# Optimization experiments

Measured on AMD Instinct MI355X. Metric: run time of the kernel, lower is better.

Reference implementation:

```python
import jax, jax.numpy as jnp
import numpy as np


def quantize_ternary(w):
    # BitNet b1.58: scale by mean |w|, round, clamp to {-1,0,1}
    gamma = jnp.maximum(jnp.mean(jnp.abs(w)), 1e-8)
    return jnp.clip(jnp.round(w / gamma), -1.0, 1.0)


def setup_inputs() -> dict:
    key = jax.random.key(0)
    k1, k2, k3 = jax.random.split(key, 3)
    in_features, out_features = 4096, 4096
    x = jax.random.normal(k1, (4, 2048, in_features), dtype=jnp.float32)
    # kaiming_uniform-like init
    bound_w = 1.0 / np.sqrt(in_features)
    weight = jax.random.uniform(k2, (out_features, in_features), dtype=jnp.float32,
                                minval=-bound_w * np.sqrt(3.0), maxval=bound_w * np.sqrt(3.0))
    bias = jax.random.uniform(k3, (out_features,), dtype=jnp.float32,
                              minval=-bound_w, maxval=bound_w)
    return {"x": x, "weight": weight, "bias": bias}


def reference(x, weight, bias):
    qw = quantize_ternary(weight)  # [out, in], values in {-1,0,1}
    # F.linear: x @ qw.T + bias
    return jnp.einsum('bsi,oi->bso', x, qw) + bias
```

## Files before the change

### kernel.cpp

```cpp
#include <hip/hip_runtime.h>
#include <stdint.h>

#define M_DIM 8192
#define N_DIM 4096
#define K_DIM 4096
#define BM 256
#define BN 256
#define BKS 64
#define NSLAB (K_DIM / BKS)
#define SLOT_BYTES (256 * BKS)

typedef int i32x4 __attribute__((ext_vector_type(4)));

__device__ __forceinline__ void async_copy16(const void* g, void* l) {
    __builtin_amdgcn_global_load_lds(
        (const __attribute__((address_space(1))) void*)g,
        (__attribute__((address_space(3))) void*)l, 16, 0, 0);
}

__global__ __launch_bounds__(256) void abssum_partial(const float4* __restrict__ w,
                                                      double* __restrict__ partials) {
    const int lane = threadIdx.x & 63;
    const int wave = threadIdx.x >> 6;
    int base = blockIdx.x * 4096 + threadIdx.x;
    float s = 0.f;
    #pragma unroll
    for (int i = 0; i < 16; i++) {
        float4 v = w[base + i * 256];
        s += fabsf(v.x) + fabsf(v.y) + fabsf(v.z) + fabsf(v.w);
    }
    double d = (double)s;
    #pragma unroll
    for (int off = 32; off > 0; off >>= 1) d += __shfl_down(d, off, 64);
    __shared__ double wsum[4];
    if (lane == 0) wsum[wave] = d;
    __syncthreads();
    if (threadIdx.x == 0)
        partials[blockIdx.x] = (wsum[0] + wsum[1]) + (wsum[2] + wsum[3]);
}

__global__ __launch_bounds__(256) void gamma_reduce(const double* __restrict__ partials,
                                                    float* __restrict__ gamma_out) {
    const int lane = threadIdx.x & 63;
    const int wave = threadIdx.x >> 6;
    double d = partials[threadIdx.x] + partials[threadIdx.x + 256] +
               partials[threadIdx.x + 512] + partials[threadIdx.x + 768];
    #pragma unroll
    for (int off = 32; off > 0; off >>= 1) d += __shfl_down(d, off, 64);
    __shared__ double wsum[4];
    if (lane == 0) wsum[wave] = d;
    __syncthreads();
    if (threadIdx.x == 0) {
        double total = (wsum[0] + wsum[1]) + (wsum[2] + wsum[3]);
        float g = (float)(total * (1.0 / 16777216.0));
        gamma_out[0] = fmaxf(g, 1e-8f);
    }
}

__global__ __launch_bounds__(256) void wquant(const float4* __restrict__ w,
                                              char4* __restrict__ qw,
                                              const float* __restrict__ gamma_p, int n4) {
    float gamma = gamma_p[0];
    int i = blockIdx.x * blockDim.x + threadIdx.x;
    if (i >= n4) return;
    float4 v = w[i];
    char4 o;
    o.x = (signed char)fminf(fmaxf(rintf(v.x / gamma), -1.f), 1.f);
    o.y = (signed char)fminf(fmaxf(rintf(v.y / gamma), -1.f), 1.f);
    o.z = (signed char)fminf(fmaxf(rintf(v.z / gamma), -1.f), 1.f);
    o.w = (signed char)fminf(fmaxf(rintf(v.w / gamma), -1.f), 1.f);
    qw[i] = o;
}

__global__ __launch_bounds__(256) void xquant(const float4* __restrict__ x,
                                              char4* __restrict__ xq,
                                              float* __restrict__ xscale) {
    const int row = blockIdx.x;
    const int lane = threadIdx.x & 63;
    const int wave = threadIdx.x >> 6;
    const float4* xr = x + (size_t)row * (K_DIM / 4);
    float4 v[4];
    float m = 0.f;
    #pragma unroll
    for (int i = 0; i < 4; i++) {
        v[i] = xr[threadIdx.x + i * 256];
        m = fmaxf(m, fmaxf(fmaxf(fabsf(v[i].x), fabsf(v[i].y)),
                           fmaxf(fabsf(v[i].z), fabsf(v[i].w))));
    }
    #pragma unroll
    for (int off = 32; off > 0; off >>= 1) m = fmaxf(m, __shfl_down(m, off, 64));
    __shared__ float wmax[4];
    if (lane == 0) wmax[wave] = m;
    __syncthreads();
    const float mx = fmaxf(fmaxf(wmax[0], wmax[1]), fmaxf(wmax[2], wmax[3]));
    const float scale = fmaxf(mx * (1.f / 127.f), 1e-30f);
    const float inv = 1.f / scale;
    if (threadIdx.x == 0) xscale[row] = scale;
    char4* oq = xq + (size_t)row * (K_DIM / 4);
    #pragma unroll
    for (int i = 0; i < 4; i++) {
        char4 o;
        o.x = (signed char)fminf(fmaxf(rintf(v[i].x * inv), -127.f), 127.f);
        o.y = (signed char)fminf(fmaxf(rintf(v[i].y * inv), -127.f), 127.f);
        o.z = (signed char)fminf(fmaxf(rintf(v[i].z * inv), -127.f), 127.f);
        o.w = (signed char)fminf(fmaxf(rintf(v[i].w * inv), -127.f), 127.f);
        oq[threadIdx.x + i * 256] = o;
    }
}

__global__ __launch_bounds__(512, 2) void gemm_kernel(
    const char* __restrict__ xq,
    const char* __restrict__ qw,
    const float* __restrict__ xscale,
    const float* __restrict__ bias,
    float* __restrict__ out)
{
    __shared__ __align__(16) char As[4][SLOT_BYTES];
    __shared__ __align__(16) char Bs[4][SLOT_BYTES];

    const int tid  = threadIdx.x;
    const int wave = tid >> 6;
    const int lane = tid & 63;
    const int wm   = (wave >> 2) * 128;
    const int wn   = (wave & 3) * 64;
    const int lm   = lane & 15;
    const int q4   = lane >> 4;

    const int bm = blockIdx.y * BM;
    const int bn = blockIdx.x * BN;

    const int rsub = lane >> 2;
    const int csw  = (lane & 3) ^ ((lane >> 3) & 3);
    const char* gA[2];
    const char* gB[2];
    int ldsOff[2];
    #pragma unroll
    for (int j = 0; j < 2; j++) {
        const int r = wave * 32 + j * 16 + rsub;
        gA[j] = xq + (size_t)(bm + r) * K_DIM + csw * 16;
        gB[j] = qw + (size_t)(bn + r) * K_DIM + csw * 16;
        ldsOff[j] = (wave * 32 + j * 16) * BKS;
    }

    i32x4 acc[8][4];
    #pragma unroll
    for (int i = 0; i < 8; i++)
        #pragma unroll
        for (int j = 0; j < 4; j++) acc[i][j] = (i32x4){0, 0, 0, 0};

    const int pc = (q4 ^ ((lm >> 1) & 3)) * 16;

    auto stage_slab = [&](int ts, int slot) {
        async_copy16(gA[0] + (size_t)ts * BKS, &As[slot][ldsOff[0]]);
        async_copy16(gB[0] + (size_t)ts * BKS, &Bs[slot][ldsOff[0]]);
        async_copy16(gA[1] + (size_t)ts * BKS, &As[slot][ldsOff[1]]);
        async_copy16(gB[1] + (size_t)ts * BKS, &Bs[slot][ldsOff[1]]);
    };

    auto compute_slab = [&](const char* Ab, const char* Bb) {
        i32x4 b[4], a[8];
        #pragma unroll
        for (int ni = 0; ni < 4; ni++)
            b[ni] = *(const i32x4*)(Bb + (wn + ni * 16 + lm) * BKS + pc);
        #pragma unroll
        for (int mi = 0; mi < 8; mi++)
            a[mi] = *(const i32x4*)(Ab + (wm + mi * 16 + lm) * BKS + pc);
        __builtin_amdgcn_s_setprio(1);
        #pragma unroll
        for (int mi = 0; mi < 8; mi++)
            #pragma unroll
            for (int ni = 0; ni < 4; ni++)
                acc[mi][ni] = __builtin_amdgcn_mfma_i32_16x16x64_i8(
                    a[mi], b[ni], acc[mi][ni], 0, 0, 0);
        __builtin_amdgcn_s_setprio(0);
    };

    #pragma unroll
    for (int s = 0; s < 3; s++) stage_slab(s, s);
    asm volatile("s_waitcnt vmcnt(8)" ::: "memory");
    __builtin_amdgcn_s_barrier();

    for (int tb = 0; tb < NSLAB - 4; tb += 4) {
        #pragma unroll
        for (int u = 0; u < 4; u++) {
            stage_slab(tb + u + 3, (u + 3) & 3);
            compute_slab(As[u], Bs[u]);
            asm volatile("s_waitcnt vmcnt(8)" ::: "memory");
            __builtin_amdgcn_s_barrier();
        }
    }

    stage_slab(63, 3);
    compute_slab(As[0], Bs[0]);
    asm volatile("s_waitcnt vmcnt(8)" ::: "memory");
    __builtin_amdgcn_s_barrier();

    compute_slab(As[1], Bs[1]);
    asm volatile("s_waitcnt vmcnt(4)" ::: "memory");
    __builtin_amdgcn_s_barrier();

    compute_slab(As[2], Bs[2]);
    asm volatile("s_waitcnt vmcnt(0)" ::: "memory");
    __builtin_amdgcn_s_barrier();

    compute_slab(As[3], Bs[3]);

    float bl[4];
    #pragma unroll
    for (int ni = 0; ni < 4; ni++) bl[ni] = bias[bn + wn + ni * 16 + lm];

    #pragma unroll
    for (int mi = 0; mi < 8; mi++) {
        #pragma unroll
        for (int r = 0; r < 4; r++) {
            const int grow = bm + wm + mi * 16 + q4 * 4 + r;
            const float sc = xscale[grow];
            float* orow = out + (size_t)grow * N_DIM + bn + wn;
            #pragma unroll
            for (int ni = 0; ni < 4; ni++)
                orow[ni * 16 + lm] = sc * (float)acc[mi][ni][r] + bl[ni];
        }
    }
}

extern "C" void kernel_launch(void* const* d_in, const int* in_sizes, int n_in,
                              void* d_out, int out_size, void* d_ws, size_t ws_size,
                              hipStream_t stream) {
    const float* x    = (const float*)d_in[0];
    const float* w    = (const float*)d_in[1];
    const float* bias = (const float*)d_in[2];
    float* out = (float*)d_out;

    char* ws = (char*)d_ws;
    char*   xq       = ws;
    char*   qw       = ws + (size_t)M_DIM * K_DIM;
    float*  xscale   = (float*)(qw + (size_t)N_DIM * K_DIM);
    double* partials = (double*)(xscale + M_DIM);
    float*  gamma_p  = (float*)(partials + 1024);

    const int wn4 = (N_DIM * K_DIM) / 4;

    abssum_partial<<<1024, 256, 0, stream>>>((const float4*)w, partials);
    gamma_reduce<<<1, 256, 0, stream>>>(partials, gamma_p);
    wquant<<<(wn4 + 255) / 256, 256, 0, stream>>>((const float4*)w, (char4*)qw, gamma_p, wn4);
    xquant<<<M_DIM, 256, 0, stream>>>((const float4*)x, (char4*)xq, xscale);

    dim3 grid(N_DIM / BN, M_DIM / BM);
    gemm_kernel<<<grid, 512, 0, stream>>>(xq, qw, xscale, bias, out);
}
```

Before: 413.6 us.

## Shrink GEMM tile to 256x128 with double buffering for higher occupancy

The int8 MFMA GEMM tile drops from 256x256 to 256x128. The LDS pipeline goes from a 4-slot ring with 3 slabs in flight to a 2-slot double buffer, and launch bounds target 4 blocks per CU instead of 2. Each wave now holds a 64x64 accumulator instead of 128x64, which frees registers and LDS so more waves fit per CU. The cost is less data reuse per loaded tile, more global traffic for the A operand, a shallower prefetch depth, and a full vmcnt(0) wait every slab.

```diff
diff --git a/kernel.cpp b/kernel.cpp
--- a/kernel.cpp
+++ b/kernel.cpp
@@ -5,10 +5,11 @@
 #define N_DIM 4096
 #define K_DIM 4096
 #define BM 256
-#define BN 256
+#define BN 128
 #define BKS 64
 #define NSLAB (K_DIM / BKS)
-#define SLOT_BYTES (256 * BKS)
+#define A_SLOT (BM * BKS)
+#define B_SLOT (BN * BKS)
 
 typedef int i32x4 __attribute__((ext_vector_type(4)));
 
@@ -108,21 +109,21 @@
     }
 }
 
-__global__ __launch_bounds__(512, 2) void gemm_kernel(
+__global__ __launch_bounds__(512, 4) void gemm_kernel(
     const char* __restrict__ xq,
     const char* __restrict__ qw,
     const float* __restrict__ xscale,
     const float* __restrict__ bias,
     float* __restrict__ out)
 {
-    __shared__ __align__(16) char As[4][SLOT_BYTES];
-    __shared__ __align__(16) char Bs[4][SLOT_BYTES];
+    __shared__ __align__(16) char As[2][A_SLOT];
+    __shared__ __align__(16) char Bs[2][B_SLOT];
 
     const int tid  = threadIdx.x;
     const int wave = tid >> 6;
     const int lane = tid & 63;
-    const int wm   = (wave >> 2) * 128;
-    const int wn   = (wave & 3) * 64;
+    const int wm   = (wave >> 1) * 64;
+    const int wn   = (wave & 1) * 64;
     const int lm   = lane & 15;
     const int q4   = lane >> 4;
 
@@ -132,42 +133,41 @@
     const int rsub = lane >> 2;
     const int csw  = (lane & 3) ^ ((lane >> 3) & 3);
     const char* gA[2];
-    const char* gB[2];
-    int ldsOff[2];
+    int ldsOffA[2];
     #pragma unroll
     for (int j = 0; j < 2; j++) {
         const int r = wave * 32 + j * 16 + rsub;
         gA[j] = xq + (size_t)(bm + r) * K_DIM + csw * 16;
-        gB[j] = qw + (size_t)(bn + r) * K_DIM + csw * 16;
-        ldsOff[j] = (wave * 32 + j * 16) * BKS;
-    }
-
-    i32x4 acc[8][4];
-    #pragma unroll
-    for (int i = 0; i < 8; i++)
+        ldsOffA[j] = (wave * 32 + j * 16) * BKS;
+    }
+    const char* gB0 = qw + (size_t)(bn + wave * 16 + rsub) * K_DIM + csw * 16;
+    const int ldsOffB = wave * 16 * BKS;
+
+    i32x4 acc[4][4];
+    #pragma unroll
+    for (int i = 0; i < 4; i++)
         #pragma unroll
         for (int j = 0; j < 4; j++) acc[i][j] = (i32x4){0, 0, 0, 0};
 
     const int pc = (q4 ^ ((lm >> 1) & 3)) * 16;
 
     auto stage_slab = [&](int ts, int slot) {
-        async_copy16(gA[0] + (size_t)ts * BKS, &As[slot][ldsOff[0]]);
-        async_copy16(gB[0] + (size_t)ts * BKS, &Bs[slot][ldsOff[0]]);
-        async_copy16(gA[1] + (size_t)ts * BKS, &As[slot][ldsOff[1]]);
-        async_copy16(gB[1] + (size_t)ts * BKS, &Bs[slot][ldsOff[1]]);
+        async_copy16(gA[0] + (size_t)ts * BKS, &As[slot][ldsOffA[0]]);
+        async_copy16(gA[1] + (size_t)ts * BKS, &As[slot][ldsOffA[1]]);
+        async_copy16(gB0   + (size_t)ts * BKS, &Bs[slot][ldsOffB]);
     };
 
     auto compute_slab = [&](const char* Ab, const char* Bb) {
-        i32x4 b[4], a[8];
+        i32x4 a[4], b[4];
         #pragma unroll
         for (int ni = 0; ni < 4; ni++)
             b[ni] = *(const i32x4*)(Bb + (wn + ni * 16 + lm) * BKS + pc);
         #pragma unroll
-        for (int mi = 0; mi < 8; mi++)
+        for (int mi = 0; mi < 4; mi++)
             a[mi] = *(const i32x4*)(Ab + (wm + mi * 16 + lm) * BKS + pc);
         __builtin_amdgcn_s_setprio(1);
         #pragma unroll
-        for (int mi = 0; mi < 8; mi++)
+        for (int mi = 0; mi < 4; mi++)
             #pragma unroll
             for (int ni = 0; ni < 4; ni++)
                 acc[mi][ni] = __builtin_amdgcn_mfma_i32_16x16x64_i8(
@@ -175,42 +175,33 @@
         __builtin_amdgcn_s_setprio(0);
     };
 
-    #pragma unroll
-    for (int s = 0; s < 3; s++) stage_slab(s, s);
-    asm volatile("s_waitcnt vmcnt(8)" ::: "memory");
-    __builtin_amdgcn_s_barrier();
-
-    for (int tb = 0; tb < NSLAB - 4; tb += 4) {
-        #pragma unroll
-        for (int u = 0; u < 4; u++) {
-            stage_slab(tb + u + 3, (u + 3) & 3);
-            compute_slab(As[u], Bs[u]);
-            asm volatile("s_waitcnt vmcnt(8)" ::: "memory");
-            __builtin_amdgcn_s_barrier();
-        }
-    }
-
-    stage_slab(63, 3);
-    compute_slab(As[0], Bs[0]);
-    asm volatile("s_waitcnt vmcnt(8)" ::: "memory");
-    __builtin_amdgcn_s_barrier();
-
-    compute_slab(As[1], Bs[1]);
-    asm volatile("s_waitcnt vmcnt(4)" ::: "memory");
-    __builtin_amdgcn_s_barrier();
-
-    compute_slab(As[2], Bs[2]);
+    stage_slab(0, 0);
     asm volatile("s_waitcnt vmcnt(0)" ::: "memory");
     __builtin_amdgcn_s_barrier();
 
-    compute_slab(As[3], Bs[3]);
+    for (int t = 0; t < NSLAB - 2; t += 2) {
+        stage_slab(t + 1, 1);
+        compute_slab(As[0], Bs[0]);
+        asm volatile("s_waitcnt vmcnt(0)" ::: "memory");
+        __builtin_amdgcn_s_barrier();
+
+        stage_slab(t + 2, 0);
+        compute_slab(As[1], Bs[1]);
+        asm volatile("s_waitcnt vmcnt(0)" ::: "memory");
+        __builtin_amdgcn_s_barrier();
+    }
+    stage_slab(NSLAB - 1, 1);
+    compute_slab(As[0], Bs[0]);
+    asm volatile("s_waitcnt vmcnt(0)" ::: "memory");
+    __builtin_amdgcn_s_barrier();
+    compute_slab(As[1], Bs[1]);
 
     float bl[4];
     #pragma unroll
     for (int ni = 0; ni < 4; ni++) bl[ni] = bias[bn + wn + ni * 16 + lm];
 
     #pragma unroll
-    for (int mi = 0; mi < 8; mi++) {
+    for (int mi = 0; mi < 4; mi++) {
         #pragma unroll
         for (int r = 0; r < 4; r++) {
             const int grow = bm + wm + mi * 16 + q4 * 4 + r;
```

Result: no change. 414.0 us (+0.1%).
